# Performance work log

Hardware: AMD Instinct MI355X
Metric: run time of the kernel (lower is better)

Reference implementation:

```python
import jax, jax.numpy as jnp
import numpy as np

N = 40000          # total samples; s pattern: first N//2 are group 0, rest group 1
TOP = 0.3          # top_percentile
LAM = 10.0
ITS = 10
P = 0.5


def setup_inputs() -> dict:
    key = jax.random.key(0)
    k1, k2 = jax.random.split(key)
    y_pred = jax.random.uniform(k1, (N,), dtype=jnp.float32)  # predicted probs in [0,1]
    # deterministic half/half sensitive attribute so group sizes are static
    s = (jnp.arange(N) >= N // 2).astype(jnp.int32)
    y_gt = jax.random.uniform(k2, (N,), dtype=jnp.float32)    # unused by forward math
    pct_a = jnp.full((1,), 0.2, dtype=jnp.float32)            # unused (threshold_based=False)
    pct_b = jnp.full((1,), 0.8, dtype=jnp.float32)            # unused
    return {"y_pred": y_pred, "s": s, "y_gt": y_gt, "pct_a": pct_a, "pct_b": pct_b}


def _wasserstein(y_pred):
    n = y_pred.shape[0]
    n0 = n // 2  # s==0 count (static: s is half zeros then half ones)
    y0 = y_pred[:n0]        # s == 0 group
    y1 = y_pred[n0:]        # s == 1 group
    nc = float(n0)
    nt = float(n - n0)
    # local_reg=True, threshold_based=False -> keep top `TOP` fraction after sort
    ia0 = int((1.0 - TOP) * n0)
    ia1 = int((1.0 - TOP) * (n - n0))
    y0 = jnp.sort(y0)[ia0:]  # (m0,)
    y1 = jnp.sort(y1)[ia1:]  # (m1,)
    m0 = y0.shape[0]
    m1 = y1.shape[0]
    # sqrt(cdist(.,p=2)**2) on 1-D points == |y1_i - y0_j|
    M = jnp.abs(y1[:, None] - y0[None, :])           # (m1, m0)
    delta = jax.lax.stop_gradient(jnp.max(M))
    eff_lam = jax.lax.stop_gradient(LAM / jnp.mean(M))
    # pad with slack row/col (delta cost, 0 in corner)
    row = delta * jnp.ones((1, m0), M.dtype)
    col = jnp.concatenate([delta * jnp.ones((m1, 1), M.dtype),
                           jnp.zeros((1, 1), M.dtype)], axis=0)
    Mt = jnp.concatenate([jnp.concatenate([M, row], axis=0), col], axis=1)  # (m1+1, m0+1)
    a = jnp.concatenate([P * jnp.ones((m1, 1), M.dtype) / nt,
                         (1.0 - P) * jnp.ones((1, 1), M.dtype)], axis=0)    # (m1+1, 1)
    b = jnp.concatenate([(1.0 - P) * jnp.ones((m0, 1), M.dtype) / nc,
                         P * jnp.ones((1, 1), M.dtype)], axis=0)            # (m0+1, 1)
    K = jnp.exp(-eff_lam * Mt) + 1e-6
    ainvK = K / a
    u = a
    for _ in range(ITS):  # fixed 10-step Sinkhorn fixed point
        u = 1.0 / (ainvK @ (b / (u.T @ K).T))
    v = b / (u.T @ K).T
    T = u * (v.T * K)
    T = jax.lax.stop_gradient(T)  # backpropT=False
    D = 2.0 * jnp.sum(T * Mt)
    return D


def reference(y_pred, s, y_gt, pct_a, pct_b):
    # s is the fixed half-zeros/half-ones pattern from setup_inputs; the static
    # slices in _wasserstein reproduce the original boolean masks exactly.
    reg_loss = _wasserstein(y_pred)
    z = jnp.zeros((1,), jnp.float32)
    return (reg_loss, z, z, z)
```

## Files before the change

kernel.cpp:

```cpp
#include <hip/hip_runtime.h>

#define HALF   20000
#define MSEL   6001
#define RANKLO 13999
#define CANDMAX 8192
#define THRESH 0.66f

#define NTHm  512
#define TPTm  24
#define NWAVE 8
#define NTOT  12002
#define NPADm 12288

#define OFF_CCNT  0
#define OFF_RANK  8
#define OFF_CANDV 16392
#define OFF_CANDI 32776

#define LXS  0
#define LYS  6144
#define LMV  12288
#define LRED 24576
#define LSC  24640
#define SOLVE_LDS_FLOATS 24656
#define SOLVE_LDS_BYTES (SOLVE_LDS_FLOATS * 4)

__device__ __forceinline__ float fexp2(float x) {
#if defined(__has_builtin)
#if __has_builtin(__builtin_amdgcn_exp2f)
  return __builtin_amdgcn_exp2f(x);
#else
  return exp2f(x);
#endif
#else
  return exp2f(x);
#endif
}

__device__ __forceinline__ float frcp(float x) {
#if defined(__has_builtin)
#if __has_builtin(__builtin_amdgcn_rcpf)
  return __builtin_amdgcn_rcpf(x);
#else
  return 1.0f / x;
#endif
#else
  return 1.0f / x;
#endif
}

#if defined(__has_builtin)
#if __has_builtin(__builtin_amdgcn_update_dpp) && __has_builtin(__builtin_amdgcn_readlane)
#define HAS_DPP 1
#endif
#endif

#ifdef HAS_DPP
template<int CTRL, int RM>
__device__ __forceinline__ float dppadd(float x) {
  int s = __builtin_amdgcn_update_dpp(0, __float_as_int(x), CTRL, RM, 0xf, false);
  return x + __int_as_float(s);
}
__device__ __forceinline__ float prefix64(float x) {
  x = dppadd<0x111, 0xf>(x);
  x = dppadd<0x112, 0xf>(x);
  x = dppadd<0x114, 0xf>(x);
  x = dppadd<0x118, 0xf>(x);
  x = dppadd<0x142, 0xa>(x);
  x = dppadd<0x143, 0xc>(x);
  return x;
}
__device__ __forceinline__ float prefixrow(float x) {
  x = dppadd<0x111, 0xf>(x);
  x = dppadd<0x112, 0xf>(x);
  x = dppadd<0x114, 0xf>(x);
  x = dppadd<0x118, 0xf>(x);
  return x;
}
__device__ __forceinline__ float sufrow(float x) {
  x = dppadd<0x101, 0xf>(x);
  x = dppadd<0x102, 0xf>(x);
  x = dppadd<0x104, 0xf>(x);
  x = dppadd<0x108, 0xf>(x);
  return x;
}
__device__ __forceinline__ float rdlane(float x, int l) {
  return __int_as_float(__builtin_amdgcn_readlane(__float_as_int(x), l));
}
#else
__device__ __forceinline__ float prefix64(float x) {
  for (int d = 1; d < 64; d <<= 1) {
    float o = __shfl_up(x, d, 64);
    if ((threadIdx.x & 63) >= d) x += o;
  }
  return x;
}
__device__ __forceinline__ float prefixrow(float x) {
  for (int d = 1; d < 16; d <<= 1) {
    float o = __shfl_up(x, d, 64);
    if ((threadIdx.x & 15) >= d) x += o;
  }
  return x;
}
__device__ __forceinline__ float sufrow(float x) {
  for (int d = 1; d < 16; d <<= 1) {
    float o = __shfl_down(x, d, 64);
    if ((threadIdx.x & 15) + d < 16) x += o;
  }
  return x;
}
__device__ __forceinline__ float rdlane(float x, int l) { return __shfl(x, l, 64); }
#endif


__global__ __launch_bounds__(512) void k_cand(const float* __restrict__ yp, int* wsI, float* wsF) {
  __shared__ int woff[8];
  __shared__ int blkbase;
  const int h = blockIdx.y;
  const int tid = threadIdx.x;
  const int wv = tid >> 6, ln = tid & 63;
  const int idx = blockIdx.x * 512 + tid;
  float v = 0.f;
  bool flag = false;
  if (idx < HALF) {
    v = yp[h * HALF + idx];
    flag = (v >= THRESH);
  }
  unsigned long long mask = __ballot(flag);
  if (ln == 0) woff[wv] = __popcll(mask);
  __syncthreads();
  if (tid == 0) {
    int s = 0;
#pragma unroll
    for (int w = 0; w < 8; ++w) { int t = woff[w]; woff[w] = s; s += t; }
    blkbase = atomicAdd(&wsI[OFF_CCNT + h], s);
  }
  __syncthreads();
  if (flag) {
    int pos = blkbase + woff[wv] + (int)__popcll(mask & ((1ull << ln) - 1ull));
    if (pos < CANDMAX) {
      wsF[OFF_CANDV + h * CANDMAX + pos] = v;
      wsI[OFF_CANDI + h * CANDMAX + pos] = idx;
      wsI[OFF_RANK + h * CANDMAX + pos] = 0;
    }
  }
}

__global__ __launch_bounds__(512) void k_rankc(const int* __restrict__ wsIc, float* wsF, int* wsI) {
  __shared__ float cv[512];
  __shared__ int ci[512];
  const int h = blockIdx.z;
  const int tid = threadIdx.x;
  const int cnt = min(wsIc[OFF_CCNT + h], CANDMAX);
  const int cb = blockIdx.y * 512;
  if (cb >= cnt) return;
  const int clen = min(512, cnt - cb);
  if (tid < clen) {
    cv[tid] = wsF[OFF_CANDV + h * CANDMAX + cb + tid];
    ci[tid] = wsIc[OFF_CANDI + h * CANDMAX + cb + tid];
  }
  __syncthreads();
  const int g = blockIdx.x * 512 + tid;
  if (g >= cnt) return;
  const float v = wsF[OFF_CANDV + h * CANDMAX + g];
  const int li = wsIc[OFF_CANDI + h * CANDMAX + g];
  int r = 0;
  for (int l = 0; l < clen; ++l) {
    float w = cv[l];
    r += (w < v || (w == v && ci[l] < li)) ? 1 : 0;
  }
  atomicAdd(&wsI[OFF_RANK + h * CANDMAX + g], r);
}


__device__ __forceinline__ float block_reduce(float v, float* red) {
  const int tid = threadIdx.x;
  __syncthreads();
  for (int d = 1; d < 64; d <<= 1) v += __shfl_xor(v, d, 64);
  if ((tid & 63) == 0) red[tid >> 6] = v;
  __syncthreads();
  float r = 0.f;
  if (tid < NWAVE) {
    r = red[tid];
    for (int d = 1; d < NWAVE; d <<= 1) r += __shfl_xor(r, d, 64);
    if (tid == 0) red[0] = r;
  }
  __syncthreads();
  return red[0];
}

__device__ __forceinline__ int bsearch_leq(const float* arr, float v) {
  int lo = 0, hi = MSEL;
  while (lo < hi) {
    int m = (lo + hi) >> 1;
    if (arr[m] <= v) lo = m + 1; else hi = m;
  }
  return lo;
}
__device__ __forceinline__ int bsearch_lt(const float* arr, float v) {
  int lo = 0, hi = MSEL;
  while (lo < hi) {
    int m = (lo + hi) >> 1;
    if (arr[m] < v) lo = m + 1; else hi = m;
  }
  return lo;
}

template<bool DO_W>
__device__ __forceinline__ void scan_core(float (&a)[TPTm], float (&b)[TPTm], float wsum,
                                          float* lds, float& GA, float& GB,
                                          int sout, int lout, float lnext) {
  float* red = lds + LRED;
  float* scal = lds + LSC;
  const int tid = threadIdx.x;
  const int wv = tid >> 6, ln = tid & 63;
  float ta = 0.f;
#pragma unroll
  for (int k = 0; k < TPTm; ++k) { float t = a[k]; a[k] = ta; ta += t; }
  float tb = 0.f;
#pragma unroll
  for (int k = TPTm - 1; k >= 0; --k) { tb += b[k]; b[k] = tb; }

  float tsA = __shfl_up(ta, 1, 64);
  if (ln == 0) tsA = 0.f;
  const float eA = prefix64(tsA);
  const float wTotA = rdlane(eA, 63) + rdlane(ta, 63);

  float tsB = __shfl_down(tb, 1, 64);
  if (ln == 63) tsB = 0.f;
  const float sRow = sufrow(tsB);
  const float r1 = rdlane(sRow, 16);
  const float r2 = rdlane(sRow, 32);
  const float r3 = rdlane(sRow, 48);
  const int row = ln >> 4;
  const float radd = (row == 0) ? (r1 + r2 + r3)
                   : (row == 1) ? (r2 + r3)
                   : (row == 2) ? r3 : 0.f;
  const float eB = sRow + radd;
  const float wTotB = rdlane(eB, 0) + rdlane(tb, 0);

  float wTotW = 0.f;
  if (DO_W) {
    float iW = prefix64(wsum);
    wTotW = rdlane(iW, 63);
  }
  if (ln == 0) {
    red[wv] = wTotA;
    red[16 + wv] = wTotB;
    if (DO_W) red[32 + wv] = wTotW;
  }
  __syncthreads();
  float tAs = (ln >= 1 && ln <= NWAVE) ? red[ln - 1] : 0.f;
  const float pAe = prefixrow(tAs);
  const float GAoff = rdlane(pAe, wv);
  float tBr = (ln < NWAVE) ? red[16 + (NWAVE - 1 - ln)] : 0.f;
  const float pBr = prefixrow(tBr);
  const float GBoff = (wv < NWAVE - 1) ? rdlane(pBr, (NWAVE - 2) - wv) : 0.f;
  if (tid == 0) {
    red[48] = rdlane(pAe, NWAVE);
    red[49] = rdlane(pBr, NWAVE - 1);
    if (DO_W) {
      float s = 0.f;
#pragma unroll
      for (int q = 0; q < NWAVE; ++q) s += red[32 + q];
      scal[sout] = s;
      scal[lout] = lnext;
    }
  }
  GA = GAoff + eA;
  GB = GBoff + eB;
  __syncthreads();
}

template<int MODE, int SRCY>
__device__ __forceinline__ void mpass(float* lds, float (&z)[TPTm],
                                      const float (&EA)[TPTm], const float (&EB)[TPTm],
                                      unsigned vmask, unsigned ymask,
                                      int sin, int lin, int sout, int lout) {
  float* scal = lds + LSC;
  const float au = 0.5f / 20000.0f;
  float cin = 0.f, lnext = 0.f;
  if (MODE) {
    const float kd = scal[2];
    float S_in, l_in;
    if (MODE == 1) { S_in = (float)MSEL * au; l_in = 0.5f; }
    else { S_in = scal[sin]; l_in = scal[lin]; }
    cin = 1e-6f * S_in + l_in * kd;
    lnext = 0.5f * frcp(kd * S_in + l_in * (1.0f + 1e-6f));
  }
  float a[TPTm], b[TPTm];
  float wsum = 0.f;
#pragma unroll
  for (int k = 0; k < TPTm; ++k) {
    bool isy = (ymask >> k) & 1u;
    bool val = (vmask >> k) & 1u;
    bool src = val && (isy == (SRCY != 0));
    float w = src ? (MODE ? au * frcp(z[k] + cin) : au) : 0.f;
    wsum += w;
    a[k] = w * EA[k];
    b[k] = w * EB[k];
  }
  float GA, GB;
  scan_core<(MODE != 0)>(a, b, wsum, lds, GA, GB, sout, lout, lnext);
#pragma unroll
  for (int k = 0; k < TPTm; ++k) {
    bool isy = (ymask >> k) & 1u;
    bool val = (vmask >> k) & 1u;
    if (val && (isy != (SRCY != 0)))
      z[k] = EB[k] * (GA + a[k]) + EA[k] * (GB + b[k]);
  }
}

__global__ __launch_bounds__(NTHm) void k_solve(const float* __restrict__ wsF,
                                                const int* __restrict__ wsI,
                                                float* __restrict__ out) {
  extern __shared__ float lds[];
  const int tid = threadIdx.x;
  float* xs = lds + LXS;
  float* ys = lds + LYS;
  float* mv = lds + LMV;
  float* red = lds + LRED;
  float* scal = lds + LSC;
  const float au = 0.5f / 20000.0f;
  const int base = tid * TPTm;

#pragma unroll
  for (int k = 0; k < 12; ++k) {
    xs[tid * 12 + k] = 1e30f;
    ys[tid * 12 + k] = 1e30f;
  }
#pragma unroll
  for (int k = 0; k < TPTm; ++k) mv[base + k] = 1e30f;
  __syncthreads();

  for (int h = 0; h < 2; ++h) {
    const int cnt = min(wsI[OFF_CCNT + h], CANDMAX);
    float* dst = h ? ys : xs;
    for (int c = tid; c < cnt; c += NTHm) {
      int full = wsI[OFF_RANK + h * CANDMAX + c] + (HALF - cnt);
      if (full >= RANKLO) dst[full - RANKLO] = wsF[OFF_CANDV + h * CANDMAX + c];
    }
  }
  __syncthreads();

  {
    const int i0 = tid * 12;
    if (i0 < MSEL) {
      int p = 0;
#pragma unroll
      for (int k = 0; k < 12; ++k) {
        int i = i0 + k;
        if (i >= MSEL) break;
        float x = xs[i];
        if (k == 0) p = bsearch_leq(ys, x);
        else { while (ys[p] <= x) ++p; }
        mv[i + p] = x;
      }
      int q = 0;
#pragma unroll
      for (int k = 0; k < 12; ++k) {
        int j = i0 + k;
        if (j >= MSEL) break;
        float y = ys[j];
        if (k == 0) q = bsearch_lt(xs, y);
        else { while (xs[q] < y) ++q; }
        mv[j + q] = -y;
      }
    }
  }
  __syncthreads();

  float vv[TPTm], z[TPTm];
  unsigned vmask = 0, ymask = 0;
#pragma unroll
  for (int k = 0; k < TPTm; ++k) {
    int g = base + k;
    float m = mv[g];
    bool val = (g < NTOT);
    bool isy = (m < 0.f);
    vv[k] = val ? fabsf(m) : 0.f;
    if (val) vmask |= (1u << k);
    if (val && isy) ymask |= (1u << k);
    z[k] = 0.f;
  }
  float bx0 = 0.f, bxl = 0.f, by0 = 0.f, byl = 0.f;
  if (tid == 0) {
    bx0 = xs[0]; bxl = xs[MSEL - 1];
    by0 = ys[0]; byl = ys[MSEL - 1];
  }

  {
    float a[TPTm], b[TPTm];
#pragma unroll
    for (int k = 0; k < TPTm; ++k) {
      bool isy = (ymask >> k) & 1u;
      a[k] = isy ? vv[k] : 0.f;
      b[k] = isy ? 1.f : 0.f;
    }
    float GA, GB;
    scan_core<false>(a, b, 0.f, lds, GA, GB, 0, 0, 0.f);
    const float PyT = red[48];
    float rs = 0.f;
#pragma unroll
    for (int k = 0; k < TPTm; ++k) {
      bool val = (vmask >> k) & 1u;
      bool isy = (ymask >> k) & 1u;
      if (val && !isy) {
        float P = GA + a[k];
        float S = GB + b[k];
        float p = (float)MSEL - S;
        rs += vv[k] * (2.f * p - (float)MSEL) + PyT - 2.f * P;
      }
    }
    float tot = block_reduce(rs, red);
    if (tid == 0) {
      float meanM = tot / ((float)MSEL * (float)MSEL);
      float lam = 10.0f / meanM;
      float lamL2 = lam * 1.4426950408889634f;
      float delta = fmaxf(byl - bx0, bxl - by0);
      float kd = fexp2(-lamL2 * delta) + 1e-6f;
      float lo = fminf(bx0, by0);
      float hi = fmaxf(bxl, byl);
      scal[0] = lamL2;
      scal[1] = delta;
      scal[2] = kd;
      scal[3] = 0.5f * (lo + hi);
    }
  }
  __syncthreads();

  const float lamL2 = scal[0];
  const float mid = scal[3];
  float EA[TPTm], EB[TPTm];
#pragma unroll
  for (int k = 0; k < TPTm; ++k) {
    if ((vmask >> k) & 1u) {
      float X = lamL2 * (vv[k] - mid);
      EA[k] = fexp2(X);
      EB[k] = fexp2(-X);
    } else { EA[k] = 0.f; EB[k] = 0.f; }
  }

  mpass<0, 1>(lds, z, EA, EB, vmask, ymask, 0, 0, 0, 0);
  mpass<1, 0>(lds, z, EA, EB, vmask, ymask, 5, 7, 4, 6);
  mpass<2, 1>(lds, z, EA, EB, vmask, ymask, 4, 6, 5, 7);
  for (int it = 1; it < 10; ++it) {
    mpass<2, 0>(lds, z, EA, EB, vmask, ymask, 5, 7, 4, 6);
    mpass<2, 1>(lds, z, EA, EB, vmask, ymask, 4, 6, 5, 7);
  }

  const float delta = scal[1], kd2 = scal[2];
  const float Sx = scal[4], Sy = scal[5], lX = scal[6], lY = scal[7];
  const float cin_v = 1e-6f * Sy + lY * kd2;
  const float cin_u = 1e-6f * Sx + lX * kd2;

  float vw[TPTm], dv[TPTm];
#pragma unroll
  for (int k = 0; k < TPTm; ++k) {
    bool val = (vmask >> k) & 1u;
    bool isy = (ymask >> k) & 1u;
    vw[k] = (val && !isy) ? au * frcp(z[k] + cin_v) : 0.f;
    dv[k] = 0.f;
  }

  float a[TPTm], b[TPTm];
  float GA, GB;
#pragma unroll
  for (int k = 0; k < TPTm; ++k) { a[k] = vw[k] * EA[k]; b[k] = vw[k] * EB[k]; }
  scan_core<false>(a, b, 0.f, lds, GA, GB, 0, 0, 0.f);
#pragma unroll
  for (int k = 0; k < TPTm; ++k) {
    if ((ymask >> k) & 1u)
      dv[k] = vv[k] * (EB[k] * (GA + a[k]) - EA[k] * (GB + b[k]));
  }
#pragma unroll
  for (int k = 0; k < TPTm; ++k) { a[k] = vw[k] * vv[k] * EA[k]; b[k] = vw[k] * vv[k] * EB[k]; }
  scan_core<false>(a, b, 0.f, lds, GA, GB, 0, 0, 0.f);
#pragma unroll
  for (int k = 0; k < TPTm; ++k) {
    if ((ymask >> k) & 1u)
      dv[k] += -EB[k] * (GA + a[k]) + EA[k] * (GB + b[k]);
  }
#pragma unroll
  for (int k = 0; k < TPTm; ++k) { a[k] = vw[k]; b[k] = vw[k] * vv[k]; }
  scan_core<false>(a, b, 0.f, lds, GA, GB, 0, 0, 0.f);
  const float Sv = red[48];
  const float TVX = red[49];
  float acc = 0.f;
#pragma unroll
  for (int k = 0; k < TPTm; ++k) {
    if ((ymask >> k) & 1u) {
      float P = GA + a[k];
      float S = GB + b[k];
      float d6 = dv[k] + 1e-6f * (vv[k] * (2.f * P - Sv) + 2.f * S - TVX);
      float u = au * frcp(z[k] + cin_u);
      acc += u * d6;
    }
  }
  float Dc = block_reduce(acc, red);
  if (tid == 0) {
    float v_last = 0.5f / (kd2 * Sy + lY * (1.0f + 1e-6f));
    float D = Dc + delta * kd2 * (lY * Sv + v_last * Sy);
    out[0] = 2.0f * D;
    out[1] = 0.f;
    out[2] = 0.f;
    out[3] = 0.f;
  }
}

extern "C" void kernel_launch(void* const* d_in, const int* in_sizes, int n_in,
                              void* d_out, int out_size, void* d_ws, size_t ws_size,
                              hipStream_t stream) {
  const float* yp = (const float*)d_in[0];
  float* wsF = (float*)d_ws;
  int* wsI = (int*)d_ws;
  float* out = (float*)d_out;

  hipMemsetAsync((char*)d_ws + OFF_CCNT * 4, 0, 8, stream);
  k_cand<<<dim3(40, 2), 512, 0, stream>>>(yp, wsI, wsF);
  k_rankc<<<dim3(16, 16, 2), 512, 0, stream>>>(wsI, wsF, wsI);
  k_solve<<<1, NTHm, SOLVE_LDS_BYTES, stream>>>(wsF, wsI, out);
}
```

Baseline: 108.9 us.

## Double solve-kernel block to 1024 threads with 12 elements per thread

Raises the single-block Sinkhorn solve kernel from 512 to 1024 threads, halving the per-thread element count, and adjusts the cross-wave scan totals for 16 waves. It also recomputes the per-element reciprocal weights in each scan pass instead of keeping them in an array, to cut register pressure. The aim is more parallel lanes on the serial scan-dominated solve. In exchange, the cross-wave prefix and the barriers now span twice as many waves, and the reciprocals are computed three times.

```diff
diff --git a/kernel.cpp b/kernel.cpp
--- a/kernel.cpp
+++ b/kernel.cpp
@@ -6,11 +6,11 @@
 #define CANDMAX 8192
 #define THRESH 0.66f
 
-#define NTHm  512
-#define TPTm  24
-#define NWAVE 8
+#define NTHm  1024
+#define TPTm  12
+#define NWAVE 16
 #define NTOT  12002
-#define NPADm 12288
+#define XPT   6
 
 #define OFF_CCNT  0
 #define OFF_RANK  8
@@ -250,14 +250,14 @@
     if (DO_W) red[32 + wv] = wTotW;
   }
   __syncthreads();
-  float tAs = (ln >= 1 && ln <= NWAVE) ? red[ln - 1] : 0.f;
+  float tAs = (ln >= 1 && ln < NWAVE) ? red[ln - 1] : 0.f;
   const float pAe = prefixrow(tAs);
   const float GAoff = rdlane(pAe, wv);
   float tBr = (ln < NWAVE) ? red[16 + (NWAVE - 1 - ln)] : 0.f;
   const float pBr = prefixrow(tBr);
   const float GBoff = (wv < NWAVE - 1) ? rdlane(pBr, (NWAVE - 2) - wv) : 0.f;
   if (tid == 0) {
-    red[48] = rdlane(pAe, NWAVE);
+    red[48] = rdlane(pAe, NWAVE - 1) + red[NWAVE - 1];
     red[49] = rdlane(pBr, NWAVE - 1);
     if (DO_W) {
       float s = 0.f;
@@ -325,9 +325,9 @@
   const int base = tid * TPTm;
 
 #pragma unroll
-  for (int k = 0; k < 12; ++k) {
-    xs[tid * 12 + k] = 1e30f;
-    ys[tid * 12 + k] = 1e30f;
+  for (int k = 0; k < XPT; ++k) {
+    xs[tid * XPT + k] = 1e30f;
+    ys[tid * XPT + k] = 1e30f;
   }
 #pragma unroll
   for (int k = 0; k < TPTm; ++k) mv[base + k] = 1e30f;
@@ -344,11 +344,11 @@
   __syncthreads();
 
   {
-    const int i0 = tid * 12;
+    const int i0 = tid * XPT;
     if (i0 < MSEL) {
       int p = 0;
 #pragma unroll
-      for (int k = 0; k < 12; ++k) {
+      for (int k = 0; k < XPT; ++k) {
         int i = i0 + k;
         if (i >= MSEL) break;
         float x = xs[i];
@@ -358,7 +358,7 @@
       }
       int q = 0;
 #pragma unroll
-      for (int k = 0; k < 12; ++k) {
+      for (int k = 0; k < XPT; ++k) {
         int j = i0 + k;
         if (j >= MSEL) break;
         float y = ys[j];
@@ -454,27 +454,29 @@
   const float cin_v = 1e-6f * Sy + lY * kd2;
   const float cin_u = 1e-6f * Sx + lX * kd2;
 
-  float vw[TPTm], dv[TPTm];
-#pragma unroll
-  for (int k = 0; k < TPTm; ++k) {
-    bool val = (vmask >> k) & 1u;
-    bool isy = (ymask >> k) & 1u;
-    vw[k] = (val && !isy) ? au * frcp(z[k] + cin_v) : 0.f;
-    dv[k] = 0.f;
-  }
-
+  float dv[TPTm];
   float a[TPTm], b[TPTm];
   float GA, GB;
 #pragma unroll
-  for (int k = 0; k < TPTm; ++k) { a[k] = vw[k] * EA[k]; b[k] = vw[k] * EB[k]; }
+  for (int k = 0; k < TPTm; ++k) {
+    bool isx = ((vmask >> k) & 1u) && !((ymask >> k) & 1u);
+    float vw = isx ? au * frcp(z[k] + cin_v) : 0.f;
+    a[k] = vw * EA[k];
+    b[k] = vw * EB[k];
+  }
   scan_core<false>(a, b, 0.f, lds, GA, GB, 0, 0, 0.f);
 #pragma unroll
   for (int k = 0; k < TPTm; ++k) {
-    if ((ymask >> k) & 1u)
-      dv[k] = vv[k] * (EB[k] * (GA + a[k]) - EA[k] * (GB + b[k]));
-  }
-#pragma unroll
-  for (int k = 0; k < TPTm; ++k) { a[k] = vw[k] * vv[k] * EA[k]; b[k] = vw[k] * vv[k] * EB[k]; }
+    dv[k] = ((ymask >> k) & 1u)
+          ? vv[k] * (EB[k] * (GA + a[k]) - EA[k] * (GB + b[k])) : 0.f;
+  }
+#pragma unroll
+  for (int k = 0; k < TPTm; ++k) {
+    bool isx = ((vmask >> k) & 1u) && !((ymask >> k) & 1u);
+    float vwx = isx ? (au * frcp(z[k] + cin_v)) * vv[k] : 0.f;
+    a[k] = vwx * EA[k];
+    b[k] = vwx * EB[k];
+  }
   scan_core<false>(a, b, 0.f, lds, GA, GB, 0, 0, 0.f);
 #pragma unroll
   for (int k = 0; k < TPTm; ++k) {
@@ -482,7 +484,12 @@
       dv[k] += -EB[k] * (GA + a[k]) + EA[k] * (GB + b[k]);
   }
 #pragma unroll
-  for (int k = 0; k < TPTm; ++k) { a[k] = vw[k]; b[k] = vw[k] * vv[k]; }
+  for (int k = 0; k < TPTm; ++k) {
+    bool isx = ((vmask >> k) & 1u) && !((ymask >> k) & 1u);
+    float vw = isx ? au * frcp(z[k] + cin_v) : 0.f;
+    a[k] = vw;
+    b[k] = vw * vv[k];
+  }
   scan_core<false>(a, b, 0.f, lds, GA, GB, 0, 0, 0.f);
   const float Sv = red[48];
   const float TVX = red[49];
```

After: 102.5 us. 1.06x faster.
